# Kernel optimization log

Measured on AMD Instinct MI355X. Metric: run time of the kernel, lower is better.

Reference implementation:

```python
import jax, jax.numpy as jnp
import numpy as np

V, D, B, L, Dh, BS = 50257, 1024, 8, 2, 128, 256

def setup_inputs() -> dict:
    key = jax.random.key(0)
    ks = jax.random.split(key, 16)
    std = lambda fan: 1.0 / np.sqrt(fan)
    return {
        'input_id': jax.random.randint(ks[0], (BS,), 0, V),
        'reset_mask': jax.random.randint(ks[1], (BS,), 0, 2).astype(bool),
        'surprise': jnp.zeros((BS, 1), jnp.float32),
        'wm_state': jax.random.normal(ks[2], (BS, D), jnp.float32) * 0.1,
        'h_state': jax.random.normal(ks[3], (L, BS, B, Dh), jnp.float32) * 0.1,
        'emb': jax.random.normal(ks[4], (V, D), jnp.float32) * std(D),
        'W_in': jax.random.normal(ks[5], (D, D), jnp.float32) * std(D),
        'W_alpha': jax.random.normal(ks[6], (D, D), jnp.float32) * std(D),
        'W_wm_out': jax.random.normal(ks[7], (D, D), jnp.float32) * std(D),
        'W_x': jax.random.normal(ks[8], (L, B, Dh, Dh), jnp.float32) * std(Dh),
        'W_h': jax.random.normal(ks[9], (L, B, Dh, Dh), jnp.float32) * std(Dh),
        'W_wml': jax.random.normal(ks[10], (L, B, Dh, D), jnp.float32) * std(D),
        'W_g': jax.random.normal(ks[11], (L, B, Dh, Dh), jnp.float32) * std(Dh),
        'w_s': jnp.zeros((L, B, Dh), jnp.float32),   # surprise gate weights (init 0, as in torch init)
        'b_g': jnp.zeros((L, B, Dh), jnp.float32),   # gate bias
    }


def reference(input_id, reset_mask, surprise, wm_state, h_state, emb, W_in,
              W_alpha, W_wm_out, W_x, W_h, W_wml, W_g, w_s, b_g):
    # carry = (~reset_mask) as float, zeroes all recurrent state at doc boundary
    carry = (~reset_mask).astype(jnp.float32)[:, None]            # [BS,1]
    x = emb[input_id]                                             # [BS,D] token embedding
    # GLA-style working memory: input-conditioned decay of carried state
    alpha = jax.nn.sigmoid(x @ W_alpha.T)                         # [BS,D]
    wm_new = carry * alpha * wm_state + x                         # [BS,D]
    y_wm = jnp.tanh(wm_new @ W_wm_out.T)                          # [BS,D]
    # input projection and split into B block slices of width D_h
    x_proj = x @ W_in.T                                           # [BS,D]
    cur = x_proj.reshape(BS, B, Dh)                               # [BS,B,Dh]
    carry_b = carry[:, :, None]                                   # [BS,1,1]
    # L sequential layers per block; all B blocks updated in parallel via einsum
    for l in range(L):
        a = (jnp.einsum('sbd,bed->sbe', cur, W_x[l])
             + jnp.einsum('sbd,bed->sbe', h_state[l], W_h[l])
             + jnp.einsum('sD,beD->sbe', y_wm, W_wml[l]))         # [BS,B,Dh]
        g = jax.nn.sigmoid(jnp.einsum('sbd,bed->sbe', a, W_g[l])
                           + surprise[:, :, None] * w_s[l] + b_g[l])
        h_new = carry_b * ((1.0 - g) * h_state[l] + g * jnp.tanh(a))
        cur = h_new
    h_final = cur.reshape(BS, D)                                  # concat of per-block outputs
    logits = h_final @ emb.T                                      # tied lm_head
    return logits, x, y_wm
```

## Files before the change

### kernel.cpp

```cpp
#include <hip/hip_runtime.h>
#include <math.h>

#define BSZ 256
#define DIM 1024
#define VOC 50257
#define NL 2
#define NB 8
#define DH 128

typedef __bf16 bf16x8 __attribute__((ext_vector_type(8)));
typedef float  f32x4  __attribute__((ext_vector_type(4)));
typedef unsigned short u16;
typedef u16 u16x8 __attribute__((ext_vector_type(8)));

__device__ __forceinline__ u16 f2bf(float f) {
  unsigned int u = __float_as_uint(f);
  u += 0x7fffu + ((u >> 16) & 1u);
  return (u16)(u >> 16);
}
__device__ __forceinline__ float sigm(float x) { return 1.0f / (1.0f + __expf(-x)); }

template<int M16, int N16, int K, bool CLAMPN>
__device__ __forceinline__ void wave_gemm(
    const u16* __restrict__ A, int lda,
    const float* __restrict__ B, int ldb, int nClamp,
    f32x4 (&acc)[M16][N16])
{
  const int lane = threadIdx.x & 63;
  const int quad = lane >> 4;
  const int l16  = lane & 15;

  const u16* aR[M16];
  const float* bR[N16];
#pragma unroll
  for (int mi = 0; mi < M16; ++mi)
    aR[mi] = A + (long)(mi * 16 + l16) * lda + quad * 8;
#pragma unroll
  for (int ni = 0; ni < N16; ++ni) {
    int n = ni * 16 + l16;
    if (CLAMPN) n = n > nClamp ? nClamp : n;
    bR[ni] = B + (long)n * ldb + quad * 8;
  }

  bf16x8 aF[2][M16];
  bf16x8 bF[2][N16];

#define WG_LOAD(kk, buf)                                                  \
  {                                                                       \
    _Pragma("unroll")                                                     \
    for (int ni = 0; ni < N16; ++ni) {                                    \
      float4 v0 = *(const float4*)(bR[ni] + (kk));                        \
      float4 v1 = *(const float4*)(bR[ni] + (kk) + 4);                    \
      u16x8 h;                                                            \
      h[0] = f2bf(v0.x); h[1] = f2bf(v0.y);                               \
      h[2] = f2bf(v0.z); h[3] = f2bf(v0.w);                               \
      h[4] = f2bf(v1.x); h[5] = f2bf(v1.y);                               \
      h[6] = f2bf(v1.z); h[7] = f2bf(v1.w);                               \
      bF[buf][ni] = __builtin_bit_cast(bf16x8, h);                        \
    }                                                                     \
    _Pragma("unroll")                                                     \
    for (int mi = 0; mi < M16; ++mi)                                      \
      aF[buf][mi] = *(const bf16x8*)(aR[mi] + (kk));                      \
  }

#define WG_MM(buf)                                                        \
  {                                                                       \
    _Pragma("unroll")                                                     \
    for (int mi = 0; mi < M16; ++mi)                                      \
      _Pragma("unroll")                                                   \
      for (int ni = 0; ni < N16; ++ni)                                    \
        acc[mi][ni] = __builtin_amdgcn_mfma_f32_16x16x32_bf16(            \
            aF[buf][mi], bF[buf][ni], acc[mi][ni], 0, 0, 0);              \
  }

  WG_LOAD(0, 0);
#pragma unroll 1
  for (int kk = 0; kk < K - 64; kk += 64) {
    WG_LOAD(kk + 32, 1);
    WG_MM(0);
    WG_LOAD(kk + 64, 0);
    WG_MM(1);
  }
  WG_LOAD(K - 32, 1);
  WG_MM(0);
  WG_MM(1);
#undef WG_LOAD
#undef WG_MM
}

#define ACC_DECL(N16V)                                \
  f32x4 acc[4][N16V];                                 \
  { f32x4 z = {0.f, 0.f, 0.f, 0.f};                   \
    _Pragma("unroll")                                 \
    for (int i = 0; i < 4; ++i)                       \
      _Pragma("unroll")                               \
      for (int j = 0; j < N16V; ++j) acc[i][j] = z; }

__global__ __launch_bounds__(256) void k_prep(
    const int* __restrict__ ids, const void* __restrict__ mask,
    const float* __restrict__ emb, const float* __restrict__ hstate,
    const float* __restrict__ W_alpha, const float* __restrict__ W_in,
    const float* __restrict__ W_wm_out, const float* __restrict__ W_x,
    const float* __restrict__ W_h, const float* __restrict__ W_wml,
    const float* __restrict__ W_g,
    float* __restrict__ xout, u16* __restrict__ x_bf,
    u16* __restrict__ h_bf, float* __restrict__ carry, float* __restrict__ sink)
{
  __shared__ int sInt;
  const int tid = threadIdx.x, s = blockIdx.x;
  if (tid == 0) sInt = 1;
  __syncthreads();
  if (tid < 64) {
    int v = ((const int*)mask)[tid];
    if (v != 0 && v != 1) atomicAnd(&sInt, 0);
  }
  __syncthreads();
  if (tid == 0) {
    int m = sInt ? ((const int*)mask)[s] : (int)((const unsigned char*)mask)[s];
    carry[s] = m ? 0.0f : 1.0f;
  }
  long id = ids[s];
  int k = tid * 4;
  float4 v = *(const float4*)(emb + id * DIM + k);
  *(float4*)(xout + (long)s * DIM + k) = v;
  ushort4 h; h.x = f2bf(v.x); h.y = f2bf(v.y); h.z = f2bf(v.z); h.w = f2bf(v.w);
  *(ushort4*)(x_bf + (long)s * DIM + k) = h;
#pragma unroll
  for (int l = 0; l < NL; ++l) {
    long off = (long)l * BSZ * DIM + (long)s * DIM + k;
    float4 w = *(const float4*)(hstate + off);
    ushort4 o; o.x = f2bf(w.x); o.y = f2bf(w.y); o.z = f2bf(w.z); o.w = f2bf(w.w);
    *(ushort4*)(h_bf + off) = o;
  }
  long gtid = (long)blockIdx.x * 256 + tid;
  long gstride = (long)gridDim.x * 256;
  float acc = 0.f;
  {
    const long nDD = (long)DIM * DIM / 4;
    for (long i = gtid; i < nDD; i += gstride) {
      float4 a = ((const float4*)W_alpha)[i];
      float4 b = ((const float4*)W_in)[i];
      float4 c = ((const float4*)W_wm_out)[i];
      acc += a.x + a.w + b.x + b.w + c.x + c.w;
    }
    const long nS = (long)NL * NB * DH * DH / 4;
    for (long i = gtid; i < nS; i += gstride) {
      float4 a = ((const float4*)W_x)[i];
      float4 b = ((const float4*)W_h)[i];
      float4 c = ((const float4*)W_g)[i];
      acc += a.x + a.w + b.x + b.w + c.x + c.w;
    }
    const long nW = (long)NL * NB * DH * DIM / 4;
    for (long i = gtid; i < nW; i += gstride) {
      float4 a = ((const float4*)W_wml)[i];
      acc += a.x + a.w;
    }
  }
  if (acc == -1.17521e35f) *sink = acc;
}

__global__ __launch_bounds__(64) void k_gemm1(
    const u16* __restrict__ x_bf,
    const float* __restrict__ W_alpha, const float* __restrict__ W_in,
    const float* __restrict__ carry, const float* __restrict__ wm_state,
    const float* __restrict__ xout,
    u16* __restrict__ wm_bf, u16* __restrict__ cur_bf)
{
  const int tid = threadIdx.x, quad = tid >> 4, l16 = tid & 15;
  const int m = blockIdx.x & 3;
  const int nt = blockIdx.x >> 2;
  const bool isAlpha = nt < 64;
  const int n0 = (isAlpha ? nt : nt - 64) * 16;
  ACC_DECL(1)
  wave_gemm<4, 1, DIM, false>(x_bf + (long)m * 64 * DIM, DIM,
                              (isAlpha ? W_alpha : W_in) + (long)n0 * DIM, DIM, 0, acc);
#pragma unroll
  for (int mi = 0; mi < 4; ++mi) {
    int n = n0 + l16;
#pragma unroll
    for (int r = 0; r < 4; ++r) {
      int s = m * 64 + mi * 16 + quad * 4 + r;
      float c = acc[mi][0][r];
      long idx = (long)s * DIM + n;
      if (isAlpha) wm_bf[idx] = f2bf(carry[s] * sigm(c) * wm_state[idx] + xout[idx]);
      else         cur_bf[idx] = f2bf(c);
    }
  }
}

__global__ __launch_bounds__(64) void k_gemm2(
    const u16* __restrict__ wm_bf, const float* __restrict__ W_wm_out,
    float* __restrict__ yout, u16* __restrict__ ywm_bf)
{
  const int tid = threadIdx.x, quad = tid >> 4, l16 = tid & 15;
  const int m = blockIdx.x & 3;
  const int n0 = (blockIdx.x >> 2) * 16;
  ACC_DECL(1)
  wave_gemm<4, 1, DIM, false>(wm_bf + (long)m * 64 * DIM, DIM,
                              W_wm_out + (long)n0 * DIM, DIM, 0, acc);
#pragma unroll
  for (int mi = 0; mi < 4; ++mi) {
    int n = n0 + l16;
#pragma unroll
    for (int r = 0; r < 4; ++r) {
      int s = m * 64 + mi * 16 + quad * 4 + r;
      float y = tanhf(acc[mi][0][r]);
      long idx = (long)s * DIM + n;
      yout[idx] = y;
      ywm_bf[idx] = f2bf(y);
    }
  }
}

__global__ __launch_bounds__(64) void k_gemm_a(
    int l, const u16* __restrict__ cur_bf, const u16* __restrict__ h_bf,
    const u16* __restrict__ ywm_bf,
    const float* __restrict__ W_x, const float* __restrict__ W_h,
    const float* __restrict__ W_wml,
    float* __restrict__ a_f32, u16* __restrict__ a_bf)
{
  const int tid = threadIdx.x, quad = tid >> 4, l16 = tid & 15;
  const int m = blockIdx.x & 3;
  const int nt = blockIdx.x >> 2;
  const int b = nt >> 3;
  const int e0 = (nt & 7) * 16;
  ACC_DECL(1)
  const long moff = (long)m * 64 * DIM;
  wave_gemm<4, 1, DH, false>(cur_bf + moff + b * DH, DIM,
                             W_x + ((long)(l * NB + b) * DH + e0) * DH, DH, 0, acc);
  wave_gemm<4, 1, DH, false>(h_bf + (long)l * BSZ * DIM + moff + b * DH, DIM,
                             W_h + ((long)(l * NB + b) * DH + e0) * DH, DH, 0, acc);
  wave_gemm<4, 1, DIM, false>(ywm_bf + moff, DIM,
                              W_wml + ((long)(l * NB + b) * DH + e0) * DIM, DIM, 0, acc);
#pragma unroll
  for (int mi = 0; mi < 4; ++mi) {
    int e = e0 + l16;
#pragma unroll
    for (int r = 0; r < 4; ++r) {
      int s = m * 64 + mi * 16 + quad * 4 + r;
      float c = acc[mi][0][r];
      long idx = (long)s * DIM + b * DH + e;
      a_f32[idx] = c;
      a_bf[idx] = f2bf(c);
    }
  }
}

__global__ __launch_bounds__(64) void k_gemm_g(
    int l, const u16* __restrict__ a_bf, const float* __restrict__ W_g,
    const float* __restrict__ w_s, const float* __restrict__ b_g,
    const float* __restrict__ surprise, const float* __restrict__ carry,
    const float* __restrict__ hstate, const float* __restrict__ a_f32,
    u16* __restrict__ hout_bf)
{
  const int tid = threadIdx.x, quad = tid >> 4, l16 = tid & 15;
  const int m = blockIdx.x & 3;
  const int nt = blockIdx.x >> 2;
  const int b = nt >> 3;
  const int e0 = (nt & 7) * 16;
  ACC_DECL(1)
  wave_gemm<4, 1, DH, false>(a_bf + (long)m * 64 * DIM + b * DH, DIM,
                             W_g + ((long)(l * NB + b) * DH + e0) * DH, DH, 0, acc);
#pragma unroll
  for (int mi = 0; mi < 4; ++mi) {
    int e = e0 + l16;
#pragma unroll
    for (int r = 0; r < 4; ++r) {
      int s = m * 64 + mi * 16 + quad * 4 + r;
      float c = acc[mi][0][r];
      long idx = (long)s * DIM + b * DH + e;
      float gp = c + surprise[s] * w_s[(l * NB + b) * DH + e] + b_g[(l * NB + b) * DH + e];
      float g = sigm(gp);
      float ho = hstate[(long)l * BSZ * DIM + idx];
      float hn = carry[s] * ((1.0f - g) * ho + g * tanhf(a_f32[idx]));
      hout_bf[idx] = f2bf(hn);
    }
  }
}

__global__ __launch_bounds__(256) void k_logits_lds(
    const u16* __restrict__ hfin_bf, const float* __restrict__ emb,
    float* __restrict__ out)
{
  __shared__ u16 Bs[2][32 * 64];
  const int tid  = threadIdx.x;
  const int wave = tid >> 6;
  const int lane = tid & 63;
  const int quad = lane >> 4;
  const int l16  = lane & 15;
  const int n0   = blockIdx.x * 32;

  const int srow = tid >> 3;
  const int scol = (tid & 7) * 8;
  long gn = n0 + srow;
  if (gn >= VOC) gn = VOC - 1;
  const float* src = emb + gn * DIM + scol;
  const int sbyte = srow * 128 + ((scol * 2) ^ ((srow & 7) << 4));

  const u16* aP[4];
#pragma unroll
  for (int mi = 0; mi < 4; ++mi)
    aP[mi] = hfin_bf + (long)(wave * 64 + mi * 16 + l16) * DIM + quad * 8;

  f32x4 acc[4][2];
  { f32x4 z = {0.f, 0.f, 0.f, 0.f};
#pragma unroll
    for (int mi = 0; mi < 4; ++mi)
#pragma unroll
      for (int ni = 0; ni < 2; ++ni) acc[mi][ni] = z; }

#define CVT_WRITE(dstbase)                                                \
  {                                                                       \
    u16x8 h8;                                                             \
    h8[0] = f2bf(pA.x); h8[1] = f2bf(pA.y);                               \
    h8[2] = f2bf(pA.z); h8[3] = f2bf(pA.w);                               \
    h8[4] = f2bf(pB.x); h8[5] = f2bf(pB.y);                               \
    h8[6] = f2bf(pB.z); h8[7] = f2bf(pB.w);                               \
    *(u16x8*)((char*)(dstbase) + sbyte) = h8;                             \
  }

  float4 pA, pB;
  pA = *(const float4*)(src);
  pB = *(const float4*)(src + 4);
  CVT_WRITE(&Bs[0][0])
  pA = *(const float4*)(src + 64);
  pB = *(const float4*)(src + 68);
  __syncthreads();

  const int NT = DIM / 64;
#pragma unroll 1
  for (int t = 0; t < NT; ++t) {
    const char* bb = (const char*)&Bs[t & 1][0];
    const int k0 = t * 64;

    bf16x8 aF0[4], aF1[4], bF0[2], bF1[2];
#pragma unroll
    for (int mi = 0; mi < 4; ++mi) aF0[mi] = *(const bf16x8*)(aP[mi] + k0);
#pragma unroll
    for (int mi = 0; mi < 4; ++mi) aF1[mi] = *(const bf16x8*)(aP[mi] + k0 + 32);
#pragma unroll
    for (int ni = 0; ni < 2; ++ni) {
      const int row = ni * 16 + l16;
      const int ib0 = (quad * 16) ^ ((row & 7) << 4);
      bF0[ni] = *(const bf16x8*)(bb + row * 128 + ib0);
      bF1[ni] = *(const bf16x8*)(bb + row * 128 + (ib0 ^ 64));
    }
#pragma unroll
    for (int mi = 0; mi < 4; ++mi)
#pragma unroll
      for (int ni = 0; ni < 2; ++ni)
        acc[mi][ni] = __builtin_amdgcn_mfma_f32_16x16x32_bf16(
            aF0[mi], bF0[ni], acc[mi][ni], 0, 0, 0);
#pragma unroll
    for (int mi = 0; mi < 4; ++mi)
#pragma unroll
      for (int ni = 0; ni < 2; ++ni)
        acc[mi][ni] = __builtin_amdgcn_mfma_f32_16x16x32_bf16(
            aF1[mi], bF1[ni], acc[mi][ni], 0, 0, 0);

    __syncthreads();
    if (t + 1 < NT) {
      CVT_WRITE(&Bs[(t + 1) & 1][0])
      if (t + 2 < NT) {
        pA = *(const float4*)(src + (t + 2) * 64);
        pB = *(const float4*)(src + (t + 2) * 64 + 4);
      }
    }
    __syncthreads();
  }
#undef CVT_WRITE

#pragma unroll
  for (int mi = 0; mi < 4; ++mi)
#pragma unroll
    for (int ni = 0; ni < 2; ++ni) {
      int n = n0 + ni * 16 + l16;
      if (n < VOC) {
#pragma unroll
        for (int r = 0; r < 4; ++r) {
          int s = wave * 64 + mi * 16 + quad * 4 + r;
          out[(long)s * VOC + n] = acc[mi][ni][r];
        }
      }
    }
}

extern "C" void kernel_launch(void* const* d_in, const int* in_sizes, int n_in,
                              void* d_out, int out_size, void* d_ws, size_t ws_size,
                              hipStream_t stream) {
  const int*   input_id = (const int*)d_in[0];
  const void*  reset    = d_in[1];
  const float* surprise = (const float*)d_in[2];
  const float* wm_state = (const float*)d_in[3];
  const float* h_state  = (const float*)d_in[4];
  const float* emb      = (const float*)d_in[5];
  const float* W_in     = (const float*)d_in[6];
  const float* W_alpha  = (const float*)d_in[7];
  const float* W_wm_out = (const float*)d_in[8];
  const float* W_x      = (const float*)d_in[9];
  const float* W_h      = (const float*)d_in[10];
  const float* W_wml    = (const float*)d_in[11];
  const float* W_g      = (const float*)d_in[12];
  const float* w_s      = (const float*)d_in[13];
  const float* b_g      = (const float*)d_in[14];

  float* out  = (float*)d_out;
  float* xout = out + (size_t)BSZ * VOC;
  float* yout = xout + (size_t)BSZ * DIM;

  const long SD = (long)BSZ * DIM;
  u16* scr    = (u16*)d_out;
  u16* x_bf   = scr;
  u16* wm_bf  = scr + SD;
  u16* cur_bf = scr + 2 * SD;
  u16* ywm_bf = scr + 3 * SD;
  u16* h_bf   = scr + 4 * SD;
  u16* a_bf   = scr + 6 * SD;
  float* a_f32 = (float*)(scr + 8 * SD);

  float* carry  = (float*)d_ws;
  u16* hfin_bf  = (u16*)((char*)d_ws + 1024);
  float* sink   = (float*)((char*)d_ws + 600 * 1024);

  k_prep<<<BSZ, 256, 0, stream>>>(input_id, reset, emb, h_state,
                                  W_alpha, W_in, W_wm_out, W_x, W_h, W_wml, W_g,
                                  xout, x_bf, h_bf, carry, sink);
  k_gemm1<<<512, 64, 0, stream>>>(x_bf, W_alpha, W_in, carry, wm_state, xout, wm_bf, cur_bf);
  k_gemm2<<<256, 64, 0, stream>>>(wm_bf, W_wm_out, yout, ywm_bf);
  k_gemm_a<<<256, 64, 0, stream>>>(0, cur_bf, h_bf, ywm_bf, W_x, W_h, W_wml, a_f32, a_bf);
  k_gemm_g<<<256, 64, 0, stream>>>(0, a_bf, W_g, w_s, b_g, surprise, carry, h_state, a_f32, cur_bf);
  k_gemm_a<<<256, 64, 0, stream>>>(1, cur_bf, h_bf, ywm_bf, W_x, W_h, W_wml, a_f32, a_bf);
  k_gemm_g<<<256, 64, 0, stream>>>(1, a_bf, W_g, w_s, b_g, surprise, carry, h_state, a_f32, hfin_bf);
  k_logits_lds<<<(VOC + 31) / 32, 256, 0, stream>>>(hfin_bf, emb, out);
}
```

Baseline: 504.8 us.

## Widen logits tile to 64 vocab rows, drop a barrier, deepen GEMM prefetch

The logits kernel now handles 64 vocabulary rows per block instead of 32. Each thread converts 16 fp32 embedding values to bf16 per stage, and each wave computes a 4x4 grid of MFMA tiles, so the A-operand (hfin) loads from global memory are amortised over twice as many columns. The LDS write for the next stage now happens before a single barrier, which removes one __syncthreads per k-step. Separately, the shared wave_gemm helper keeps four register buffers in flight instead of two, giving more prefetch depth. In exchange, register pressure goes up in both paths and the number of logits blocks is halved, which may reduce occupancy.

```diff
diff --git a/kernel.cpp b/kernel.cpp
--- a/kernel.cpp
+++ b/kernel.cpp
@@ -42,8 +42,8 @@
     bR[ni] = B + (long)n * ldb + quad * 8;
   }
 
-  bf16x8 aF[2][M16];
-  bf16x8 bF[2][N16];
+  bf16x8 aF[4][M16];
+  bf16x8 bF[4][N16];
 
 #define WG_LOAD(kk, buf)                                                  \
   {                                                                       \
@@ -74,16 +74,17 @@
   }
 
   WG_LOAD(0, 0);
+  WG_LOAD(32, 1);
+  WG_LOAD(64, 2);
 #pragma unroll 1
-  for (int kk = 0; kk < K - 64; kk += 64) {
-    WG_LOAD(kk + 32, 1);
-    WG_MM(0);
-    WG_LOAD(kk + 64, 0);
-    WG_MM(1);
-  }
-  WG_LOAD(K - 32, 1);
-  WG_MM(0);
-  WG_MM(1);
+  for (int kk = 0; kk < K - 128; kk += 128) {
+    WG_LOAD(kk + 96, 3);  WG_MM(0);
+    WG_LOAD(kk + 128, 0); WG_MM(1);
+    WG_LOAD(kk + 160, 1); WG_MM(2);
+    WG_LOAD(kk + 192, 2); WG_MM(3);
+  }
+  WG_LOAD(K - 32, 3);
+  WG_MM(0); WG_MM(1); WG_MM(2); WG_MM(3);
 #undef WG_LOAD
 #undef WG_MM
 }
@@ -282,49 +283,57 @@
     const u16* __restrict__ hfin_bf, const float* __restrict__ emb,
     float* __restrict__ out)
 {
-  __shared__ u16 Bs[2][32 * 64];
+  __shared__ u16 Bs[2][64 * 64];
   const int tid  = threadIdx.x;
   const int wave = tid >> 6;
   const int lane = tid & 63;
   const int quad = lane >> 4;
   const int l16  = lane & 15;
-  const int n0   = blockIdx.x * 32;
-
-  const int srow = tid >> 3;
-  const int scol = (tid & 7) * 8;
+  const int n0   = blockIdx.x * 64;
+
+  const int srow = tid >> 2;
+  const int scol = (tid & 3) * 16;
   long gn = n0 + srow;
   if (gn >= VOC) gn = VOC - 1;
   const float* src = emb + gn * DIM + scol;
-  const int sbyte = srow * 128 + ((scol * 2) ^ ((srow & 7) << 4));
+  const int sw  = (srow & 7) << 4;
+  const int sb0 = srow * 128 + ((scol * 2) ^ sw);
+  const int sb1 = srow * 128 + (((scol * 2) + 16) ^ sw);
 
   const u16* aP[4];
 #pragma unroll
   for (int mi = 0; mi < 4; ++mi)
     aP[mi] = hfin_bf + (long)(wave * 64 + mi * 16 + l16) * DIM + quad * 8;
 
-  f32x4 acc[4][2];
+  f32x4 acc[4][4];
   { f32x4 z = {0.f, 0.f, 0.f, 0.f};
 #pragma unroll
     for (int mi = 0; mi < 4; ++mi)
 #pragma unroll
-      for (int ni = 0; ni < 2; ++ni) acc[mi][ni] = z; }
-
-#define CVT_WRITE(dstbase)                                                \
-  {                                                                       \
-    u16x8 h8;                                                             \
-    h8[0] = f2bf(pA.x); h8[1] = f2bf(pA.y);                               \
-    h8[2] = f2bf(pA.z); h8[3] = f2bf(pA.w);                               \
-    h8[4] = f2bf(pB.x); h8[5] = f2bf(pB.y);                               \
-    h8[6] = f2bf(pB.z); h8[7] = f2bf(pB.w);                               \
-    *(u16x8*)((char*)(dstbase) + sbyte) = h8;                             \
-  }
-
-  float4 pA, pB;
-  pA = *(const float4*)(src);
-  pB = *(const float4*)(src + 4);
-  CVT_WRITE(&Bs[0][0])
-  pA = *(const float4*)(src + 64);
-  pB = *(const float4*)(src + 68);
+      for (int ni = 0; ni < 4; ++ni) acc[mi][ni] = z; }
+
+  float4 pA, pB, pC, pD;
+#define LD4(t)                                                            \
+  { pA = *(const float4*)(src + (t) * 64);                                \
+    pB = *(const float4*)(src + (t) * 64 + 4);                            \
+    pC = *(const float4*)(src + (t) * 64 + 8);                            \
+    pD = *(const float4*)(src + (t) * 64 + 12); }
+#define CVT_WR(bufi)                                                      \
+  { u16x8 h0, h1;                                                         \
+    h0[0] = f2bf(pA.x); h0[1] = f2bf(pA.y);                               \
+    h0[2] = f2bf(pA.z); h0[3] = f2bf(pA.w);                               \
+    h0[4] = f2bf(pB.x); h0[5] = f2bf(pB.y);                               \
+    h0[6] = f2bf(pB.z); h0[7] = f2bf(pB.w);                               \
+    h1[0] = f2bf(pC.x); h1[1] = f2bf(pC.y);                               \
+    h1[2] = f2bf(pC.z); h1[3] = f2bf(pC.w);                               \
+    h1[4] = f2bf(pD.x); h1[5] = f2bf(pD.y);                               \
+    h1[6] = f2bf(pD.z); h1[7] = f2bf(pD.w);                               \
+    *(u16x8*)((char*)&Bs[bufi][0] + sb0) = h0;                            \
+    *(u16x8*)((char*)&Bs[bufi][0] + sb1) = h1; }
+
+  LD4(0)
+  CVT_WR(0)
+  LD4(1)
   __syncthreads();
 
   const int NT = DIM / 64;
@@ -333,13 +342,13 @@
     const char* bb = (const char*)&Bs[t & 1][0];
     const int k0 = t * 64;
 
-    bf16x8 aF0[4], aF1[4], bF0[2], bF1[2];
+    bf16x8 aF0[4], aF1[4], bF0[4], bF1[4];
 #pragma unroll
     for (int mi = 0; mi < 4; ++mi) aF0[mi] = *(const bf16x8*)(aP[mi] + k0);
 #pragma unroll
     for (int mi = 0; mi < 4; ++mi) aF1[mi] = *(const bf16x8*)(aP[mi] + k0 + 32);
 #pragma unroll
-    for (int ni = 0; ni < 2; ++ni) {
+    for (int ni = 0; ni < 4; ++ni) {
       const int row = ni * 16 + l16;
       const int ib0 = (quad * 16) ^ ((row & 7) << 4);
       bF0[ni] = *(const bf16x8*)(bb + row * 128 + ib0);
@@ -348,32 +357,29 @@
 #pragma unroll
     for (int mi = 0; mi < 4; ++mi)
 #pragma unroll
-      for (int ni = 0; ni < 2; ++ni)
+      for (int ni = 0; ni < 4; ++ni)
         acc[mi][ni] = __builtin_amdgcn_mfma_f32_16x16x32_bf16(
             aF0[mi], bF0[ni], acc[mi][ni], 0, 0, 0);
 #pragma unroll
     for (int mi = 0; mi < 4; ++mi)
 #pragma unroll
-      for (int ni = 0; ni < 2; ++ni)
+      for (int ni = 0; ni < 4; ++ni)
         acc[mi][ni] = __builtin_amdgcn_mfma_f32_16x16x32_bf16(
             aF1[mi], bF1[ni], acc[mi][ni], 0, 0, 0);
 
+    if (t + 1 < NT) {
+      CVT_WR((t + 1) & 1)
+      if (t + 2 < NT) LD4(t + 2)
+    }
     __syncthreads();
-    if (t + 1 < NT) {
-      CVT_WRITE(&Bs[(t + 1) & 1][0])
-      if (t + 2 < NT) {
-        pA = *(const float4*)(src + (t + 2) * 64);
-        pB = *(const float4*)(src + (t + 2) * 64 + 4);
-      }
-    }
-    __syncthreads();
-  }
-#undef CVT_WRITE
+  }
+#undef LD4
+#undef CVT_WR
 
 #pragma unroll
   for (int mi = 0; mi < 4; ++mi)
 #pragma unroll
-    for (int ni = 0; ni < 2; ++ni) {
+    for (int ni = 0; ni < 4; ++ni) {
       int n = n0 + ni * 16 + l16;
       if (n < VOC) {
 #pragma unroll
@@ -431,5 +437,5 @@
   k_gemm_g<<<256, 64, 0, stream>>>(0, a_bf, W_g, w_s, b_g, surprise, carry, h_state, a_f32, cur_bf);
   k_gemm_a<<<256, 64, 0, stream>>>(1, cur_bf, h_bf, ywm_bf, W_x, W_h, W_wml, a_f32, a_bf);
   k_gemm_g<<<256, 64, 0, stream>>>(1, a_bf, W_g, w_s, b_g, surprise, carry, h_state, a_f32, hfin_bf);
-  k_logits_lds<<<(VOC + 31) / 32, 256, 0, stream>>>(hfin_bf, emb, out);
-}
+  k_logits_lds<<<(VOC + 63) / 64, 256, 0, stream>>>(hfin_bf, emb, out);
+}
```

Result: faster. 461.1 us (-8.7%).
